# Kernel tuning notes

Hardware: AMD Instinct MI355X
Metric: run time of the kernel (lower is better)

The kernel has to match this reference:

```python
import jax, jax.numpy as jnp
import numpy as np

N_NODES = 100000


def gcn_conv(h_in, W, b, src, dst, ew, n_nodes):
    """PyG GCNConv: x' = D^{-1/2} (A + I) D^{-1/2} (x W) + b, with edge weights."""
    h = h_in @ W  # [N, F_out]
    loop = jnp.arange(n_nodes, dtype=src.dtype)
    row = jnp.concatenate([src, loop])            # sources (j)
    col = jnp.concatenate([dst, loop])            # targets (i)
    w = jnp.concatenate([ew, jnp.ones((n_nodes,), dtype=ew.dtype)])
    deg = jax.ops.segment_sum(w, col, num_segments=n_nodes)  # weighted in-degree incl. self-loops
    dinv = jnp.where(deg > 0, jax.lax.rsqrt(deg), 0.0)
    norm = dinv[row] * w * dinv[col]              # [E+N]
    msg = h[row] * norm[:, None]                  # gather + scale, [E+N, F_out]
    out = jax.ops.segment_sum(msg, col, num_segments=n_nodes)  # scatter to targets
    return out + b


def setup_inputs() -> dict:
    key = jax.random.key(0)
    k = jax.random.split(key, 6)
    N, E, F_in, F_hid = N_NODES, 3200000, 128, 64
    x = jax.random.normal(k[0], (N, F_in), dtype=jnp.float32)
    edge_index = jax.random.randint(k[1], (2, E), 0, N, dtype=jnp.int64)
    edge_weight = jax.random.uniform(k[2], (E,), dtype=jnp.float32)
    W1 = jax.random.normal(k[3], (F_in, F_hid), dtype=jnp.float32) * 0.1
    b1 = jnp.zeros((F_hid,), dtype=jnp.float32)
    W2 = jax.random.normal(k[4], (F_hid, 1), dtype=jnp.float32) * 0.1
    b2 = jnp.zeros((1,), dtype=jnp.float32)
    return {"x": x, "edge_index": edge_index, "edge_weight": edge_weight,
            "W1": W1, "b1": b1, "W2": W2, "b2": b2}


def reference(x, edge_index, edge_weight, W1, b1, W2, b2):
    n_nodes = x.shape[0]
    src, dst = edge_index[0], edge_index[1]
    h = jax.nn.relu(gcn_conv(x, W1, b1, src, dst, edge_weight, n_nodes))
    h = gcn_conv(h, W2, b2, src, dst, edge_weight, n_nodes)  # [N, 1]
    score = jax.nn.sigmoid(h)[:, 0]
    # degree-weighted scoring (original edges, no self-loops), scatter onto source
    deg_weighted = jax.ops.segment_sum(edge_weight, src, num_segments=n_nodes)
    deg_norm = deg_weighted / jnp.max(deg_weighted)
    return score * (1.0 + deg_norm)
```

## Files before the change

kernel.cpp:

```cpp
#include <hip/hip_runtime.h>
#include <hip/hip_fp16.h>
#include <math.h>

#define F_IN 128
#define F_HID 64
#define NWG 256
#define PT 1024
#define BSH 7
#define BSZ 128
#define BSHS 10
#define BSZS 1024
#define SEGCAP 6144

typedef float f32x2 __attribute__((ext_vector_type(2)));
typedef float f32x4 __attribute__((ext_vector_type(4)));
typedef __bf16 bf16x8 __attribute__((ext_vector_type(8)));

__device__ __forceinline__ unsigned char f32_to_fp8(float v) {
  unsigned r = __builtin_amdgcn_cvt_pk_fp8_f32(v, v, 0, false);
  return (unsigned char)(r & 0xFFu);
}

__device__ __forceinline__ __bf16 f32_bf16(float f) {
  unsigned u = __float_as_uint(f);
  unsigned r = (u + 0x7FFFu + ((u >> 16) & 1u)) >> 16;
  return __builtin_bit_cast(__bf16, (unsigned short)r);
}

__global__ void k_count(const int* __restrict__ src, const int* __restrict__ dst,
                        int* __restrict__ cntAll, int NBD, int NBS, int E) {
  extern __shared__ int sh[];
  int* hD = sh;
  int* hS = sh + NBD;
  int tid = threadIdx.x, w = blockIdx.x;
  for (int k = tid; k < NBD + NBS; k += PT) sh[k] = 0;
  __syncthreads();
  int C = (E + NWG - 1) / NWG;
  int e0 = w * C, e1 = min(E, e0 + C);
  for (int e = e0 + tid; e < e1; e += PT) {
    atomicAdd(&hD[dst[e] >> BSH], 1);
    atomicAdd(&hS[src[e] >> BSHS], 1);
  }
  __syncthreads();
  for (int b = tid; b < NBD; b += PT) cntAll[b * NWG + w] = hD[b];
  for (int b = tid; b < NBS; b += PT) cntAll[(NBD + b) * NWG + w] = hS[b];
}

__global__ void k_scanA(int* __restrict__ data, int* __restrict__ partials, int TOT) {
  __shared__ int lds[1024];
  int tid = threadIdx.x;
  int g = blockIdx.x * 1024 + tid;
  int v = (g < TOT) ? data[g] : 0;
  lds[tid] = v; __syncthreads();
  for (int o = 1; o < 1024; o <<= 1) {
    int t = (tid >= o) ? lds[tid - o] : 0;
    __syncthreads();
    lds[tid] += t;
    __syncthreads();
  }
  if (g < TOT) data[g] = lds[tid] - v;
  if (tid == 1023) partials[blockIdx.x] = lds[1023];
}

__global__ void k_scanB(int* partials, int nb, unsigned* maxbits) {
  __shared__ int lds[1024];
  int tid = threadIdx.x;
  if (tid == 0) *maxbits = 0u;
  int v = (tid < nb) ? partials[tid] : 0;
  lds[tid] = v; __syncthreads();
  for (int o = 1; o < 1024; o <<= 1) {
    int t = (tid >= o) ? lds[tid - o] : 0;
    __syncthreads();
    lds[tid] += t;
    __syncthreads();
  }
  if (tid < nb) partials[tid] = lds[tid] - v;
}

__global__ void k_scanC(int* __restrict__ data, const int* __restrict__ partials, int TOT) {
  int g = blockIdx.x * 1024 + threadIdx.x;
  if (g < TOT) data[g] += partials[g >> 10];
}

__global__ void k_part(const int* __restrict__ src, const int* __restrict__ dst,
                       const float* __restrict__ ew, const int* __restrict__ baseAll,
                       int2* __restrict__ gD, unsigned* __restrict__ gS,
                       int NBD, int NBS, int E) {
  extern __shared__ int sh[];
  int* cD = sh;
  int* cS = sh + NBD;
  int tid = threadIdx.x, w = blockIdx.x;
  for (int b = tid; b < NBD; b += PT) cD[b] = baseAll[b * NWG + w];
  for (int b = tid; b < NBS; b += PT) cS[b] = baseAll[(NBD + b) * NWG + w] - E;
  __syncthreads();
  int C = (E + NWG - 1) / NWG;
  int e0 = w * C, e1 = min(E, e0 + C);
  for (int e = e0 + tid; e < e1; e += PT) {
    int s = src[e], d = dst[e];
    float wv = ew[e];
    int pD = atomicAdd(&cD[d >> BSH], 1);
    gD[pD] = make_int2(s | ((d & (BSZ - 1)) << 24), __float_as_int(wv));
    int pS = atomicAdd(&cS[s >> BSHS], 1);
    gS[pS] = ((unsigned)(s & (BSZS - 1)) << 16) | (unsigned)__half_as_ushort(__float2half(wv));
  }
}

__global__ void k_csr(int2* __restrict__ gD, const int* __restrict__ baseAll,
                      int* __restrict__ off, float* __restrict__ dinv,
                      int NBD, int N, int E) {
  __shared__ int2 seg[SEGCAP];
  __shared__ int hist[BSZ];
  __shared__ int curs[BSZ];
  __shared__ float degf[BSZ];
  int tid = threadIdx.x, b = blockIdx.x;
  int bstart = baseAll[b * NWG];
  int bend = (b + 1 < NBD) ? baseAll[(b + 1) * NWG] : E;
  int cnt = bend - bstart;
  for (int k = tid; k < cnt; k += 256) seg[k] = gD[bstart + k];
  if (tid < BSZ) { hist[tid] = 0; degf[tid] = 0.f; }
  __syncthreads();
  for (int k = tid; k < cnt; k += 256) {
    int dl = seg[k].x >> 24;
    atomicAdd(&hist[dl], 1);
    atomicAdd(&degf[dl], __int_as_float(seg[k].y));
  }
  __syncthreads();
  int v = (tid < BSZ) ? hist[tid] : 0;
  for (int o = 1; o < BSZ; o <<= 1) {
    int t = (tid < BSZ && tid >= o) ? hist[tid - o] : 0;
    __syncthreads();
    if (tid < BSZ) hist[tid] += t;
    __syncthreads();
  }
  if (tid < BSZ) {
    int excl = hist[tid] - v;
    curs[tid] = excl;
    int node = b * BSZ + tid;
    if (node < N) {
      off[node] = bstart + excl;
      dinv[node] = rsqrtf(1.0f + degf[tid]);
    }
  }
  if (b == NBD - 1 && tid == 0) off[N] = E;
  __syncthreads();
  for (int k = tid; k < cnt; k += 256) {
    int2 ev = seg[k];
    int dl = ev.x >> 24;
    int slot = atomicAdd(&curs[dl], 1);
    gD[bstart + slot] = make_int2(ev.x & 0xFFFFFF, ev.y);
  }
}

__global__ void k_dw(const unsigned* __restrict__ gS, const int* __restrict__ baseAll,
                     float* __restrict__ dw, unsigned* maxbits,
                     int NBD, int NBS, int N, int E) {
  __shared__ float acc[BSZS];
  int tid = threadIdx.x, b = blockIdx.x;
  int bstart = baseAll[(NBD + b) * NWG] - E;
  int bend = (b + 1 < NBS) ? baseAll[(NBD + b + 1) * NWG] - E : E;
  acc[tid] = 0.f;
  __syncthreads();
  for (int k = bstart + tid; k < bend; k += BSZS) {
    unsigned p = gS[k];
    atomicAdd(&acc[p >> 16], __half2float(__ushort_as_half((unsigned short)(p & 0xFFFFu))));
  }
  __syncthreads();
  float m = 0.f;
  int node = b * BSZS + tid;
  if (node < N) { dw[node] = acc[tid]; m = acc[tid]; }
  for (int mm = 32; mm; mm >>= 1) m = fmaxf(m, __shfl_xor(m, mm, 64));
  if ((tid & 63) == 0) atomicMax(maxbits, __float_as_uint(m));
}

__global__ void k_gemm1(const float* __restrict__ x, const float* __restrict__ W1,
                        const float* __restrict__ dinv, unsigned char* __restrict__ g0, int N) {
  int lane = threadIdx.x & 63;
  int wid = (blockIdx.x * blockDim.x + threadIdx.x) >> 6;
  int nw = (gridDim.x * blockDim.x) >> 6;
  int l16 = lane & 15, lh = lane >> 4;
  bf16x8 bfrag[4][4];
#pragma unroll
  for (int cb = 0; cb < 4; ++cb)
#pragma unroll
    for (int kf = 0; kf < 4; ++kf)
#pragma unroll
      for (int i = 0; i < 8; ++i) {
        int k = kf * 32 + lh * 8 + i;
        bfrag[cb][kf][i] = f32_bf16(W1[k * F_HID + cb * 16 + l16]);
      }
  int ntiles = (N + 15) >> 4;
  for (int t = wid; t < ntiles; t += nw) {
    int rowbase = t << 4;
    int row = min(rowbase + l16, N - 1);
    bf16x8 afrag[4];
#pragma unroll
    for (int kf = 0; kf < 4; ++kf) {
      const f32x4* xp = (const f32x4*)(x + (size_t)row * F_IN + kf * 32 + lh * 8);
      f32x4 v0 = xp[0], v1 = xp[1];
#pragma unroll
      for (int i = 0; i < 4; ++i) afrag[kf][i] = f32_bf16(v0[i]);
#pragma unroll
      for (int i = 0; i < 4; ++i) afrag[kf][4 + i] = f32_bf16(v1[i]);
    }
    f32x4 acc[4] = {{0.f,0.f,0.f,0.f},{0.f,0.f,0.f,0.f},{0.f,0.f,0.f,0.f},{0.f,0.f,0.f,0.f}};
#pragma unroll
    for (int cb = 0; cb < 4; ++cb)
#pragma unroll
      for (int kf = 0; kf < 4; ++kf)
        acc[cb] = __builtin_amdgcn_mfma_f32_16x16x32_bf16(afrag[kf], bfrag[cb][kf], acc[cb], 0, 0, 0);
    if (rowbase + 16 <= N) {
      f32x4 dv = *(const f32x4*)(dinv + rowbase + lh * 4);
#pragma unroll
      for (int cb = 0; cb < 4; ++cb)
#pragma unroll
        for (int r = 0; r < 4; ++r) {
          int rr = rowbase + lh * 4 + r;
          g0[(size_t)rr * F_HID + cb * 16 + l16] = f32_to_fp8(acc[cb][r] * dv[r]);
        }
    } else {
#pragma unroll
      for (int cb = 0; cb < 4; ++cb)
#pragma unroll
        for (int r = 0; r < 4; ++r) {
          int rr = rowbase + lh * 4 + r;
          if (rr < N)
            g0[(size_t)rr * F_HID + cb * 16 + l16] = f32_to_fp8(acc[cb][r] * dinv[rr]);
        }
    }
  }
}

__global__ void k_agg1(const unsigned char* __restrict__ g0, const float* __restrict__ dinv,
                       const int* __restrict__ off, const int2* __restrict__ csr,
                       const float* __restrict__ b1, const float* __restrict__ W2,
                       float* __restrict__ u, int N) {
  int lane = threadIdx.x & 63;
  int grp = lane >> 3;
  int l8  = lane & 7;
  int i = (blockIdx.x * blockDim.x + threadIdx.x) >> 6;
  if (i >= N) return;
  const uint2* g0v = (const uint2*)g0;
  f32x2 acc2[4] = {{0.f,0.f},{0.f,0.f},{0.f,0.f},{0.f,0.f}};
  if (grp == 0) {
    uint2 rv = g0v[(size_t)i * 8 + l8];
    acc2[0] += __builtin_amdgcn_cvt_pk_f32_fp8(rv.x, false);
    acc2[1] += __builtin_amdgcn_cvt_pk_f32_fp8(rv.x, true);
    acc2[2] += __builtin_amdgcn_cvt_pk_f32_fp8(rv.y, false);
    acc2[3] += __builtin_amdgcn_cvt_pk_f32_fp8(rv.y, true);
  }
  int p0 = off[i], p1 = off[i + 1];
  for (int p = p0; p < p1; p += 64) {
    int m = min(p1 - p, 64);
    int2 ed = make_int2(0, 0);
    if (lane < m) ed = csr[p + lane];
#pragma unroll
    for (int jj = 0; jj < 8; ++jj) {
      int j = jj * 8 + grp;
      int s = __shfl(ed.x, j, 64);
      float w = __int_as_float(__shfl(ed.y, j, 64));
      if (j < m) {
        uint2 rv = g0v[(size_t)s * 8 + l8];
        f32x2 w2; w2.x = w; w2.y = w;
        acc2[0] = __builtin_elementwise_fma(__builtin_amdgcn_cvt_pk_f32_fp8(rv.x, false), w2, acc2[0]);
        acc2[1] = __builtin_elementwise_fma(__builtin_amdgcn_cvt_pk_f32_fp8(rv.x, true),  w2, acc2[1]);
        acc2[2] = __builtin_elementwise_fma(__builtin_amdgcn_cvt_pk_f32_fp8(rv.y, false), w2, acc2[2]);
        acc2[3] = __builtin_elementwise_fma(__builtin_amdgcn_cvt_pk_f32_fp8(rv.y, true),  w2, acc2[3]);
      }
    }
  }
  float acc[8] = {acc2[0].x, acc2[0].y, acc2[1].x, acc2[1].y,
                  acc2[2].x, acc2[2].y, acc2[3].x, acc2[3].y};
#pragma unroll
  for (int k = 0; k < 8; ++k) {
    acc[k] += __shfl_xor(acc[k], 8, 64);
    acc[k] += __shfl_xor(acc[k], 16, 64);
    acc[k] += __shfl_xor(acc[k], 32, 64);
  }
  float di = dinv[i];
  float pdt = 0.f;
#pragma unroll
  for (int k = 0; k < 8; ++k) {
    int f = l8 * 8 + k;
    float h = fmaxf(di * acc[k] + b1[f], 0.f);
    pdt = fmaf(h, W2[f], pdt);
  }
  pdt += __shfl_xor(pdt, 1, 64);
  pdt += __shfl_xor(pdt, 2, 64);
  pdt += __shfl_xor(pdt, 4, 64);
  if (lane == 0) u[i] = di * pdt;
}

__global__ void k_agg2_final(const float* __restrict__ u, const float* __restrict__ dinv,
                             const int* __restrict__ off, const int2* __restrict__ csr,
                             const float* __restrict__ b2, const float* __restrict__ dw,
                             const unsigned* __restrict__ maxbits,
                             float* __restrict__ out, int N) {
  int lane32 = threadIdx.x & 31;
  int i = blockIdx.x * 8 + (threadIdx.x >> 5);
  if (i >= N) return;
  float acc = (lane32 == 0) ? u[i] : 0.f;
  int p0 = off[i], p1 = off[i + 1];
  for (int p = p0 + lane32; p < p1; p += 32) {
    int2 ed = csr[p];
    acc = fmaf(__int_as_float(ed.y), u[ed.x], acc);
  }
  for (int mm = 16; mm; mm >>= 1) acc += __shfl_xor(acc, mm, 64);
  if (lane32 == 0) {
    float md = __uint_as_float(*maxbits);
    float z = dinv[i] * acc + b2[0];
    float sc = 1.0f / (1.0f + expf(-z));
    out[i] = sc * (1.0f + dw[i] / md);
  }
}

extern "C" void kernel_launch(void* const* d_in, const int* in_sizes, int n_in,
                              void* d_out, int out_size, void* d_ws, size_t ws_size,
                              hipStream_t stream) {
  const float* x  = (const float*)d_in[0];
  const int*   ei = (const int*)d_in[1];
  const float* ew = (const float*)d_in[2];
  const float* W1 = (const float*)d_in[3];
  const float* b1 = (const float*)d_in[4];
  const float* W2 = (const float*)d_in[5];
  const float* b2 = (const float*)d_in[6];
  float* out = (float*)d_out;

  int N = out_size;
  int E = in_sizes[2];
  const int* src = ei;
  const int* dst = ei + E;

  int NBD = (N + BSZ - 1) >> BSH;
  int NBS = (N + BSZS - 1) >> BSHS;
  int TOT = (NBD + NBS) * NWG;
  int SB = (TOT + 1023) >> 10;
  size_t shmem = (size_t)(NBD + NBS) * sizeof(int);

  char* w8 = (char*)d_ws;
  int2*     gD      = (int2*)w8;
  unsigned* gS      = (unsigned*)(gD + E);
  int*      cntAll  = (int*)(gS + E);
  int*      partials= cntAll + TOT;
  int*      off     = partials + 1024;
  float*    dinv    = (float*)(off + N + 1);
  float*    dw      = dinv + N;
  float*    u       = dw + N;
  unsigned* maxbits = (unsigned*)(u + N);
  unsigned char* g0 = (unsigned char*)(maxbits + 2);

  k_count<<<NWG, PT, shmem, stream>>>(src, dst, cntAll, NBD, NBS, E);
  k_scanA<<<SB, 1024, 0, stream>>>(cntAll, partials, TOT);
  k_scanB<<<1, 1024, 0, stream>>>(partials, SB, maxbits);
  k_scanC<<<SB, 1024, 0, stream>>>(cntAll, partials, TOT);
  k_part<<<NWG, PT, shmem, stream>>>(src, dst, ew, cntAll, gD, gS, NBD, NBS, E);
  k_csr<<<NBD, 256, 0, stream>>>(gD, cntAll, off, dinv, NBD, N, E);
  k_dw<<<NBS, BSZS, 0, stream>>>(gS, cntAll, dw, maxbits, NBD, NBS, N, E);
  k_gemm1<<<256, 256, 0, stream>>>(x, W1, dinv, g0, N);
  k_agg1<<<(N * 64 + 255) / 256, 256, 0, stream>>>(g0, dinv, off, gD, b1, W2, u, N);
  k_agg2_final<<<(N + 7) / 8, 256, 0, stream>>>(u, dinv, off, gD, b2, dw, maxbits, out, N);
}
```

Measured before the change: 269.7 us.

## Stage destination partition writes through LDS to coalesce global scatter

The partition kernel now processes each block's edge range in sub-chunks of 6144 edges. Each sub-chunk is first counted per destination bucket, then locally sorted into shared memory by bucket with a block-wide scan, and finally written to global memory in bucket-contiguous runs. The aim is to replace random 8-byte scattered stores to gD with mostly contiguous writes. The cost is extra passes over src/dst, many more barriers per chunk, a large static LDS footprint that limits occupancy, and hardcoded array sizes (784/104) that assume the current N.

Result: no change. 266.7 us (-1.1%).

```diff
diff --git a/kernel.cpp b/kernel.cpp
--- a/kernel.cpp
+++ b/kernel.cpp
@@ -11,6 +11,7 @@
 #define BSHS 10
 #define BSZS 1024
 #define SEGCAP 6144
+#define SUBC 6144
 
 typedef float f32x2 __attribute__((ext_vector_type(2)));
 typedef float f32x4 __attribute__((ext_vector_type(4)));
@@ -82,26 +83,63 @@
   if (g < TOT) data[g] += partials[g >> 10];
 }
 
-__global__ void k_part(const int* __restrict__ src, const int* __restrict__ dst,
-                       const float* __restrict__ ew, const int* __restrict__ baseAll,
-                       int2* __restrict__ gD, unsigned* __restrict__ gS,
-                       int NBD, int NBS, int E) {
-  extern __shared__ int sh[];
-  int* cD = sh;
-  int* cS = sh + NBD;
+__global__ void __launch_bounds__(PT) k_part(
+    const int* __restrict__ src, const int* __restrict__ dst,
+    const float* __restrict__ ew, const int* __restrict__ baseAll,
+    int2* __restrict__ gD, unsigned* __restrict__ gS,
+    int NBD, int NBS, int E) {
+  __shared__ int2 seg[SUBC];
+  __shared__ unsigned short bkt[SUBC];
+  __shared__ int cD[784];
+  __shared__ int cS[104];
+  __shared__ int excl[784];
+  __shared__ int lcur[784];
+  __shared__ int scanT[1024];
   int tid = threadIdx.x, w = blockIdx.x;
   for (int b = tid; b < NBD; b += PT) cD[b] = baseAll[b * NWG + w];
   for (int b = tid; b < NBS; b += PT) cS[b] = baseAll[(NBD + b) * NWG + w] - E;
   __syncthreads();
   int C = (E + NWG - 1) / NWG;
   int e0 = w * C, e1 = min(E, e0 + C);
-  for (int e = e0 + tid; e < e1; e += PT) {
-    int s = src[e], d = dst[e];
-    float wv = ew[e];
-    int pD = atomicAdd(&cD[d >> BSH], 1);
-    gD[pD] = make_int2(s | ((d & (BSZ - 1)) << 24), __float_as_int(wv));
-    int pS = atomicAdd(&cS[s >> BSHS], 1);
-    gS[pS] = ((unsigned)(s & (BSZS - 1)) << 16) | (unsigned)__half_as_ushort(__float2half(wv));
+  for (int c0 = e0; c0 < e1; c0 += SUBC) {
+    int cnt = min(SUBC, e1 - c0);
+    for (int b = tid; b < NBD; b += PT) lcur[b] = 0;
+    __syncthreads();
+    for (int k = tid; k < cnt; k += PT) {
+      int e = c0 + k;
+      int s = src[e], d = dst[e];
+      atomicAdd(&lcur[d >> BSH], 1);
+      int pS = atomicAdd(&cS[s >> BSHS], 1);
+      gS[pS] = ((unsigned)(s & (BSZS - 1)) << 16) | (unsigned)__half_as_ushort(__float2half(ew[e]));
+    }
+    __syncthreads();
+    int v = (tid < NBD) ? lcur[tid] : 0;
+    scanT[tid] = v;
+    __syncthreads();
+    for (int o = 1; o < 1024; o <<= 1) {
+      int t = (tid >= o) ? scanT[tid - o] : 0;
+      __syncthreads();
+      scanT[tid] += t;
+      __syncthreads();
+    }
+    if (tid < NBD) { excl[tid] = scanT[tid] - v; lcur[tid] = scanT[tid] - v; }
+    __syncthreads();
+    for (int k = tid; k < cnt; k += PT) {
+      int e = c0 + k;
+      int s = src[e], d = dst[e];
+      int b = d >> BSH;
+      int slot = atomicAdd(&lcur[b], 1);
+      seg[slot] = make_int2(s | ((d & (BSZ - 1)) << 24), __float_as_int(ew[e]));
+      bkt[slot] = (unsigned short)b;
+    }
+    __syncthreads();
+    for (int k = tid; k < cnt; k += PT) {
+      int b = bkt[k];
+      gD[cD[b] + (k - excl[b])] = seg[k];
+    }
+    __syncthreads();
+    for (int b = tid; b < NBD; b += PT) cD[b] += lcur[b] - excl[b];
+    __syncthreads();
   }
 }
 
@@ -352,7 +390,7 @@
   k_scanA<<<SB, 1024, 0, stream>>>(cntAll, partials, TOT);
   k_scanB<<<1, 1024, 0, stream>>>(partials, SB, maxbits);
   k_scanC<<<SB, 1024, 0, stream>>>(cntAll, partials, TOT);
-  k_part<<<NWG, PT, shmem, stream>>>(src, dst, ew, cntAll, gD, gS, NBD, NBS, E);
+  k_part<<<NWG, PT, 0, stream>>>(src, dst, ew, cntAll, gD, gS, NBD, NBS, E);
   k_csr<<<NBD, 256, 0, stream>>>(gD, cntAll, off, dinv, NBD, N, E);
   k_dw<<<NBS, BSZS, 0, stream>>>(gS, cntAll, dw, maxbits, NBD, NBS, N, E);
   k_gemm1<<<256, 256, 0, stream>>>(x, W1, dinv, g0, N);
```
